# Kernel tuning notes

Measured on AMD Instinct MI355X. Metric: run time of the kernel, lower is better.

Reference implementation:

```python
import jax, jax.numpy as jnp
import numpy as np

LEAKY_SLOPE = 0.01
BN_EPS = 1e-5


def _local_conv(x, w, b, stride):
    # x: [B,C,H,W]; w: [1,O,C,OH,OW,K] (K = kh*kw, kh==kw); b: [1,O,OH,OW]
    sh, sw = stride
    _, O, C, oh, ow, K = w.shape
    k = int(round(K ** 0.5))
    # gather unfold patches: torch .unfold(2,kh,dh).unfold(3,kw,dw) -> last dim ordered (i major, j minor)
    patches = jnp.stack(
        [x[:, :, i:i + sh * oh:sh, j:j + sw * ow:sw] for i in range(k) for j in range(k)],
        axis=-1)  # [B,C,oh,ow,K]
    out = jnp.einsum('bchwk,ochwk->bohw', patches, w[0])
    return out + b  # b broadcasts [1,O,OH,OW]


def _bn_train(x, gamma, beta):
    # BatchNorm2d in training mode: biased batch statistics over (N,H,W)
    m = jnp.mean(x, axis=(0, 2, 3), keepdims=True)
    v = jnp.var(x, axis=(0, 2, 3), keepdims=True)
    return gamma[None, :, None, None] * (x - m) * jax.lax.rsqrt(v + BN_EPS) + beta[None, :, None, None]


def _lrelu(x):
    return jnp.where(x >= 0, x, LEAKY_SLOPE * x)


def _pad1(x):
    return jnp.pad(x, ((0, 0), (0, 0), (1, 1), (1, 1)))


def setup_inputs() -> dict:
    key = jax.random.key(0)
    ks = jax.random.split(key, 16)
    B = 8192
    inp = {
        'image': jax.random.normal(ks[0], (B, 10, 9, 1), jnp.float32),
        'conv1_w': jax.random.normal(ks[1], (64, 1, 2, 2), jnp.float32) * 0.5,
        'conv1_b': jax.random.normal(ks[2], (64,), jnp.float32) * 0.1,
        'lc1_w': jax.random.normal(ks[3], (1, 16, 64, 10, 5, 9), jnp.float32) * 0.05,
        'lc1_b': jax.random.normal(ks[4], (1, 16, 10, 5), jnp.float32) * 0.1,
        'lc2_w': jax.random.normal(ks[5], (1, 8, 16, 11, 6, 4), jnp.float32) * 0.1,
        'lc2_b': jax.random.normal(ks[6], (1, 8, 11, 6), jnp.float32) * 0.1,
        'lc3_w': jax.random.normal(ks[7], (1, 8, 8, 12, 4, 4), jnp.float32) * 0.1,
        'lc3_b': jax.random.normal(ks[8], (1, 8, 12, 4), jnp.float32) * 0.1,
        'gamma1': jax.random.normal(ks[9], (16,), jnp.float32) * 0.1 + 1.0,
        'beta1': jax.random.normal(ks[10], (16,), jnp.float32) * 0.1,
        'gamma2': jax.random.normal(ks[11], (8,), jnp.float32) * 0.1 + 1.0,
        'beta2': jax.random.normal(ks[12], (8,), jnp.float32) * 0.1,
        'gamma3': jax.random.normal(ks[13], (8,), jnp.float32) * 0.1 + 1.0,
        'beta3': jax.random.normal(ks[14], (8,), jnp.float32) * 0.1,
    }
    return inp


def reference(image, conv1_w, conv1_b, lc1_w, lc1_b, lc2_w, lc2_b, lc3_w, lc3_b,
              gamma1, beta1, gamma2, beta2, gamma3, beta3):
    x = jnp.transpose(image, (0, 3, 1, 2))  # [B,1,10,9]
    # Conv2d kernel 2, padding='same' (torch pads extra on right/bottom for even kernels)
    x = jax.lax.conv_general_dilated(
        x, conv1_w, window_strides=(1, 1), padding=[(0, 1), (0, 1)],
        dimension_numbers=('NCHW', 'OIHW', 'NCHW'))
    x = x + conv1_b[None, :, None, None]
    x = _lrelu(x)
    x = _pad1(x)                               # [B,64,12,11]
    x = _local_conv(x, lc1_w, lc1_b, (1, 2))   # [B,16,10,5]
    x = _lrelu(x)
    x = _bn_train(x, gamma1, beta1)
    x = _pad1(x)                               # [B,16,12,7]
    x = _local_conv(x, lc2_w, lc2_b, (1, 1))   # [B,8,11,6]
    x = _lrelu(x)
    x = _bn_train(x, gamma2, beta2)
    x = _pad1(x)                               # [B,8,13,8]
    x = _local_conv(x, lc3_w, lc3_b, (1, 2))   # [B,8,12,4]
    x = _lrelu(x)
    x = _bn_train(x, gamma3, beta3)
    return x.reshape(x.shape[0], -1)           # [B,384]
```

## Files before the change

### kernel.cpp

```cpp
#include <hip/hip_runtime.h>


typedef float  f32x4 __attribute__((ext_vector_type(4)));
typedef float  f32x2 __attribute__((ext_vector_type(2)));
typedef short  bf16x8 __attribute__((ext_vector_type(8)));

union FR  { int4 i4; bf16x8 bf; unsigned u[4]; };
union F2U { f32x2 v; unsigned u[2]; };

#define LRELU(v) fmaxf((v), 0.01f * (v))

static __device__ inline unsigned bfr(float f) {
    unsigned u = __float_as_uint(f);
    return (u + 0x7fffu + ((u >> 16) & 1u)) >> 16;
}
static __device__ inline unsigned short bfr16(float f) { return (unsigned short)bfr(f); }
static __device__ inline float ubf(unsigned lo16) { return __uint_as_float(lo16 << 16); }

#if __has_builtin(__builtin_elementwise_fma)
static __device__ inline f32x2 pk_fma(f32x2 a, f32x2 b, f32x2 c) { return __builtin_elementwise_fma(a, b, c); }
#else
static __device__ inline f32x2 pk_fma(f32x2 a, f32x2 b, f32x2 c) { return a * b + c; }
#endif
static __device__ inline f32x2 pk_lrelu(f32x2 v) {
#if __has_builtin(__builtin_elementwise_max)
    return __builtin_elementwise_max(v, v * 0.01f);
#else
    f32x2 r; r.x = LRELU(v.x); r.y = LRELU(v.y); return r;
#endif
}
static __device__ inline float aload(float* p) {
    return __hip_atomic_load(p, __ATOMIC_RELAXED, __HIP_MEMORY_SCOPE_AGENT);
}

__global__ __launch_bounds__(256) void kB_frags(
    const float* __restrict__ lw1,
    int4* __restrict__ afg1, float* __restrict__ stats)
{
    const int bx = blockIdx.x, tid = threadIdx.x;
    if (bx == 50) { if (tid < 64) stats[tid] = 0.0f; return; }

    const int pos = bx;
    __shared__ float wt[9216];
    for (int e = tid; e < 9216; e += 256) {
        int pair = e / 9, t = e - 9 * pair;
        wt[e] = lw1[pair * 450 + pos * 9 + t];
    }
    __syncthreads();
    for (int e = tid; e < 1152; e += 256) {
        int l = e & 63, ht = e >> 6;
        int h = (ht >= 9) ? 1 : 0, t = ht - 9 * h;
        int q = l >> 4, o = l & 15;
        unsigned uu[4];
        #pragma unroll
        for (int p = 0; p < 4; ++p) {
            int c0 = 32 * h + 8 * q + 2 * p;
            float w0 = wt[(o * 64 + c0) * 9 + t];
            float w1 = wt[(o * 64 + c0 + 1) * 9 + t];
            uu[p] = bfr(w0) | (bfr(w1) << 16);
        }
        int4 st = { (int)uu[0], (int)uu[1], (int)uu[2], (int)uu[3] };
        afg1[pos * 1152 + e] = st;
    }
}

__global__ __launch_bounds__(256) void k1_lc1(
    const float* __restrict__ img,
    const float* __restrict__ cw,
    const float* __restrict__ cb,
    const int4* __restrict__ afg,
    const float* __restrict__ lb,
    unsigned short* __restrict__ y1b,
    float* __restrict__ stats)
{
    __shared__ int4   AfL[1152];
    __shared__ float4 cw4s[64];
    __shared__ float  cbl[64];
    __shared__ float  bl[16];
    __shared__ float  red[32];

    const int pos = blockIdx.y;
    const int oh = pos / 5, ow = pos % 5;
    const int tid = threadIdx.x;
    const int wv = tid >> 6, lane = tid & 63;
    const int lane15 = lane & 15, q = lane >> 4;

    for (int e = tid; e < 1152; e += 256) AfL[e] = afg[pos * 1152 + e];
    if (tid < 64) { cw4s[tid] = ((const float4*)cw)[tid]; cbl[tid] = cb[tid]; }
    if (tid < 16) bl[tid] = lb[tid * 50 + pos];
    if (tid < 32) red[tid] = 0.0f;
    __syncthreads();

    bool km[9];
    #pragma unroll
    for (int i = 0; i < 3; i++)
        #pragma unroll
        for (int j = 0; j < 3; j++) {
            int r = oh + i - 1, c2 = 2 * ow + j - 1;
            km[i * 3 + j] = (r >= 0 && r < 10 && c2 >= 0 && c2 < 9);
        }

    const int sBase = blockIdx.x * 256 + wv * 64;
    float ip[4][16];
    #pragma unroll
    for (int g = 0; g < 4; ++g) {
        const float* ib = img + (size_t)(sBase + g * 16 + lane15) * 90;
        #pragma unroll
        for (int a = 0; a < 4; ++a) {
            int r = oh - 1 + a;
            bool rok = (r >= 0 && r < 10);
            #pragma unroll
            for (int d = 0; d < 4; ++d) {
                int c2 = 2 * ow - 1 + d;
                ip[g][a * 4 + d] = (rok && c2 >= 0 && c2 < 9) ? ib[r * 9 + c2] : 0.0f;
            }
        }
    }

    f32x4 acc[4];
    #pragma unroll
    for (int g = 0; g < 4; ++g) acc[g] = (f32x4){0.f, 0.f, 0.f, 0.f};

    #pragma unroll
    for (int h = 0; h < 2; ++h) {
        f32x2 wx2[4], wy2[4], wz2[4], ww2[4], cb2[4];
        #pragma unroll
        for (int p = 0; p < 4; ++p) {
            float4 wa = cw4s[h * 32 + q * 8 + 2 * p];
            float4 wb = cw4s[h * 32 + q * 8 + 2 * p + 1];
            wx2[p] = (f32x2){wa.x, wb.x};
            wy2[p] = (f32x2){wa.y, wb.y};
            wz2[p] = (f32x2){wa.z, wb.z};
            ww2[p] = (f32x2){wa.w, wb.w};
            cb2[p] = (f32x2){cbl[h * 32 + q * 8 + 2 * p], cbl[h * 32 + q * 8 + 2 * p + 1]};
        }
        #pragma unroll
        for (int t = 0; t < 9; ++t) {
            const int ti = t / 3, tj = t % 3;
            const int i0 = ti * 4 + tj;
            if (km[t]) {
                FR fa; fa.i4 = AfL[(h * 9 + t) * 64 + lane];
                #pragma unroll
                for (int g = 0; g < 4; ++g) {
                    f32x2 s0 = (f32x2)ip[g][i0];
                    f32x2 s1 = (f32x2)ip[g][i0 + 1];
                    f32x2 s2 = (f32x2)ip[g][i0 + 4];
                    f32x2 s3 = (f32x2)ip[g][i0 + 5];
                    FR fb;
                    #pragma unroll
                    for (int p = 0; p < 4; ++p) {
                        f32x2 v = pk_fma(s0, wx2[p], cb2[p]);
                        v = pk_fma(s1, wy2[p], v);
                        v = pk_fma(s2, wz2[p], v);
                        v = pk_fma(s3, ww2[p], v);
                        v = pk_lrelu(v);
                        F2U uu; uu.v = v;
                        fb.u[p] = __builtin_amdgcn_perm(uu.u[1], uu.u[0], 0x07060302u);
                    }
                    acc[g] = __builtin_amdgcn_mfma_f32_16x16x32_bf16(fa.bf, fb.bf, acc[g], 0, 0, 0);
                }
            }
        }
    }

    float so[4] = {0, 0, 0, 0}, sq[4] = {0, 0, 0, 0};
    #pragma unroll
    for (int g = 0; g < 4; ++g)
        #pragma unroll
        for (int r = 0; r < 4; ++r) {
            int o = q * 4 + r;
            float v = acc[g][r] + bl[o];
            v = LRELU(v);
            y1b[(size_t)(o * 50 + pos) * 8192 + sBase + g * 16 + lane15] = bfr16(v);
            so[r] += v; sq[r] += v * v;
        }
    #pragma unroll
    for (int r = 0; r < 4; ++r) {
        #pragma unroll
        for (int m = 1; m < 16; m <<= 1) {
            so[r] += __shfl_xor(so[r], m, 16);
            sq[r] += __shfl_xor(sq[r], m, 16);
        }
        if (lane15 == 0) {
            int o = q * 4 + r;
            atomicAdd(&red[o], so[r]);
            atomicAdd(&red[16 + o], sq[r]);
        }
    }
    __syncthreads();
    if (tid < 32) atomicAdd(&stats[tid], red[tid]);
}

__global__ __launch_bounds__(256) void k2_lc2(
    const unsigned short* __restrict__ y1b,
    const float* __restrict__ lw2, const float* __restrict__ lb2,
    const float* __restrict__ g1, const float* __restrict__ be1,
    unsigned short* __restrict__ y2b, float* __restrict__ stats)
{
    __shared__ float wld[512];
    __shared__ float a1[16], b1[16], bl[8], red[16];

    const int unit = blockIdx.x;
    const int pos = unit >> 3, chunk = unit & 7;
    const int oh = pos / 6, ow = pos % 6;
    const int tid = threadIdx.x, lane = tid & 63;

    if (tid < 128) {
        const float* src = lw2 + tid * 264 + pos * 4;
        int o = tid >> 4, c = tid & 15;
        #pragma unroll
        for (int k = 0; k < 4; k++) wld[c * 32 + k * 8 + o] = src[k];
    }
    if (tid < 16) {
        float m = aload(&stats[tid]) * (1.0f / 409600.0f);
        float v = aload(&stats[16 + tid]) * (1.0f / 409600.0f) - m * m;
        float a = g1[tid] * rsqrtf(v + 1e-5f);
        a1[tid] = a; b1[tid] = be1[tid] - a * m;
        if (tid < 8) bl[tid] = lb2[tid * 66 + pos];
        red[tid] = 0.0f;
    }
    __syncthreads();

    int base[4]; float kmv[4];
    #pragma unroll
    for (int i = 0; i < 2; i++)
        #pragma unroll
        for (int j = 0; j < 2; j++) {
            int r = oh + i - 1, c2 = ow + j - 1;
            bool ok = (r >= 0 && r < 10 && c2 >= 0 && c2 < 5);
            int rc = min(max(r, 0), 9), cc2 = min(max(c2, 0), 4);
            base[i * 2 + j] = rc * 5 + cc2;
            kmv[i * 2 + j] = ok ? 1.0f : 0.0f;
        }

    const int sb = chunk * 1024 + tid * 4;
    float acc[8][4];
    #pragma unroll
    for (int o = 0; o < 8; o++)
        #pragma unroll
        for (int s = 0; s < 4; s++) acc[o][s] = bl[o];

    #pragma unroll 1
    for (int c = 0; c < 16; c++) {
        float av = a1[c], bv = b1[c];
        float p[4][4];
        #pragma unroll
        for (int t = 0; t < 4; t++) {
            float ap = av * kmv[t], bp = bv * kmv[t];
            uint2 U = *(const uint2*)(y1b + (size_t)(c * 50 + base[t]) * 8192 + sb);
            p[t][0] = fmaf(ap, ubf(U.x & 0xffffu), bp);
            p[t][1] = fmaf(ap, __uint_as_float(U.x & 0xffff0000u), bp);
            p[t][2] = fmaf(ap, ubf(U.y & 0xffffu), bp);
            p[t][3] = fmaf(ap, __uint_as_float(U.y & 0xffff0000u), bp);
        }
        const float4* wr = (const float4*)&wld[c * 32];
        #pragma unroll
        for (int t = 0; t < 4; t++) {
            float4 wa = wr[t * 2], wb = wr[t * 2 + 1];
            #pragma unroll
            for (int s = 0; s < 4; s++) {
                float pv = p[t][s];
                acc[0][s] += wa.x * pv; acc[1][s] += wa.y * pv;
                acc[2][s] += wa.z * pv; acc[3][s] += wa.w * pv;
                acc[4][s] += wb.x * pv; acc[5][s] += wb.y * pv;
                acc[6][s] += wb.z * pv; acc[7][s] += wb.w * pv;
            }
        }
    }

    #pragma unroll
    for (int o = 0; o < 8; o++) {
        float v0 = LRELU(acc[o][0]), v1 = LRELU(acc[o][1]);
        float v2 = LRELU(acc[o][2]), v3 = LRELU(acc[o][3]);
        uint2 st = { bfr(v0) | (bfr(v1) << 16), bfr(v2) | (bfr(v3) << 16) };
        *(uint2*)(y2b + (size_t)(o * 66 + pos) * 8192 + sb) = st;
        float sv = v0 + v1 + v2 + v3;
        float sqv = v0 * v0 + v1 * v1 + v2 * v2 + v3 * v3;
        #pragma unroll
        for (int m = 32; m > 0; m >>= 1) {
            sv  += __shfl_xor(sv, m, 64);
            sqv += __shfl_xor(sqv, m, 64);
        }
        if (lane == 0) { atomicAdd(&red[o], sv); atomicAdd(&red[8 + o], sqv); }
    }
    __syncthreads();
    if (tid < 16) atomicAdd(&stats[32 + tid], red[tid]);
}

__global__ __launch_bounds__(256) void k3_lc3(
    const unsigned short* __restrict__ y2b,
    const float* __restrict__ lw3, const float* __restrict__ lb3,
    const float* __restrict__ g2, const float* __restrict__ be2,
    unsigned short* __restrict__ y3b, float* __restrict__ stats)
{
    __shared__ float wld[256];
    __shared__ float a2[8], b2[8], bl[8], red[16];

    const int unit = blockIdx.x;
    const int pos = unit >> 3, chunk = unit & 7;
    const int oh = pos >> 2, ow = pos & 3;
    const int tid = threadIdx.x, lane = tid & 63;

    if (tid < 64) {
        const float* src = lw3 + tid * 192 + pos * 4;
        int o = tid >> 3, c = tid & 7;
        #pragma unroll
        for (int k = 0; k < 4; k++) wld[c * 32 + k * 8 + o] = src[k];
    }
    if (tid < 16) {
        if (tid < 8) {
            float m = aload(&stats[32 + tid]) * (1.0f / 540672.0f);
            float v = aload(&stats[40 + tid]) * (1.0f / 540672.0f) - m * m;
            float a = g2[tid] * rsqrtf(v + 1e-5f);
            a2[tid] = a; b2[tid] = be2[tid] - a * m;
            bl[tid] = lb3[tid * 48 + pos];
        }
        red[tid] = 0.0f;
    }
    __syncthreads();

    int base[4]; float kmv[4];
    #pragma unroll
    for (int i = 0; i < 2; i++)
        #pragma unroll
        for (int j = 0; j < 2; j++) {
            int r = oh + i - 1, c2 = 2 * ow + j - 1;
            bool ok = (r >= 0 && r < 11 && c2 >= 0 && c2 < 6);
            int rc = min(max(r, 0), 10), cc2 = min(max(c2, 0), 5);
            base[i * 2 + j] = rc * 6 + cc2;
            kmv[i * 2 + j] = ok ? 1.0f : 0.0f;
        }

    const int sb = chunk * 1024 + tid * 4;
    float acc[8][4];
    #pragma unroll
    for (int o = 0; o < 8; o++)
        #pragma unroll
        for (int s = 0; s < 4; s++) acc[o][s] = bl[o];

    #pragma unroll 1
    for (int c = 0; c < 8; c++) {
        float av = a2[c], bv = b2[c];
        float p[4][4];
        #pragma unroll
        for (int t = 0; t < 4; t++) {
            float ap = av * kmv[t], bp = bv * kmv[t];
            uint2 U = *(const uint2*)(y2b + (size_t)(c * 66 + base[t]) * 8192 + sb);
            p[t][0] = fmaf(ap, ubf(U.x & 0xffffu), bp);
            p[t][1] = fmaf(ap, __uint_as_float(U.x & 0xffff0000u), bp);
            p[t][2] = fmaf(ap, ubf(U.y & 0xffffu), bp);
            p[t][3] = fmaf(ap, __uint_as_float(U.y & 0xffff0000u), bp);
        }
        const float4* wr = (const float4*)&wld[c * 32];
        #pragma unroll
        for (int t = 0; t < 4; t++) {
            float4 wa = wr[t * 2], wb = wr[t * 2 + 1];
            #pragma unroll
            for (int s = 0; s < 4; s++) {
                float pv = p[t][s];
                acc[0][s] += wa.x * pv; acc[1][s] += wa.y * pv;
                acc[2][s] += wa.z * pv; acc[3][s] += wa.w * pv;
                acc[4][s] += wb.x * pv; acc[5][s] += wb.y * pv;
                acc[6][s] += wb.z * pv; acc[7][s] += wb.w * pv;
            }
        }
    }

    #pragma unroll
    for (int o = 0; o < 8; o++) {
        float v0 = LRELU(acc[o][0]), v1 = LRELU(acc[o][1]);
        float v2 = LRELU(acc[o][2]), v3 = LRELU(acc[o][3]);
        uint2 st = { bfr(v0) | (bfr(v1) << 16), bfr(v2) | (bfr(v3) << 16) };
        *(uint2*)(y3b + (size_t)(o * 48 + pos) * 8192 + sb) = st;
        float sv = v0 + v1 + v2 + v3;
        float sqv = v0 * v0 + v1 * v1 + v2 * v2 + v3 * v3;
        #pragma unroll
        for (int m = 32; m > 0; m >>= 1) {
            sv  += __shfl_xor(sv, m, 64);
            sqv += __shfl_xor(sqv, m, 64);
        }
        if (lane == 0) { atomicAdd(&red[o], sv); atomicAdd(&red[8 + o], sqv); }
    }
    __syncthreads();
    if (tid < 16) atomicAdd(&stats[48 + tid], red[tid]);
}

__global__ __launch_bounds__(256) void k4_out(
    const unsigned short* __restrict__ y3b,
    const float* __restrict__ g3, const float* __restrict__ be3,
    float* __restrict__ stats, float* __restrict__ out)
{
    __shared__ unsigned short tile[64][66];
    __shared__ float a3[8], b3[8];
    const int unit = blockIdx.x;
    const int tid = threadIdx.x;
    const int chunkS = unit & 31, yy = unit >> 5;
    const int ftile = yy >> 2, sub = yy & 3;
    const int fbase = ftile * 64;
    const int sbase = chunkS * 256 + sub * 64;

    if (tid < 8) {
        float m = aload(&stats[48 + tid]) * (1.0f / 393216.0f);
        float v = aload(&stats[56 + tid]) * (1.0f / 393216.0f) - m * m;
        float a = g3[tid] * rsqrtf(v + 1e-5f);
        a3[tid] = a; b3[tid] = be3[tid] - a * m;
    }
    __syncthreads();

    #pragma unroll
    for (int rep = 0; rep < 16; rep++) {
        int idx = rep * 256 + tid;
        int f = idx >> 6, s = idx & 63;
        tile[f][s] = y3b[(size_t)(fbase + f) * 8192 + sbase + s];
    }
    __syncthreads();
    #pragma unroll
    for (int rep = 0; rep < 16; rep++) {
        int idx = rep * 256 + tid;
        int s = idx >> 6, f = idx & 63;
        int ff = fbase + f;
        int o = ff / 48;
        float x = ubf((unsigned)tile[f][s]);
        out[(size_t)(sbase + s) * 384 + ff] = a3[o] * x + b3[o];
    }
}

extern "C" void kernel_launch(void* const* d_in, const int* in_sizes, int n_in,
                              void* d_out, int out_size, void* d_ws, size_t ws_size,
                              hipStream_t stream) {
    const float* image   = (const float*)d_in[0];
    const float* conv1_w = (const float*)d_in[1];
    const float* conv1_b = (const float*)d_in[2];
    const float* lc1_w   = (const float*)d_in[3];
    const float* lc1_b   = (const float*)d_in[4];
    const float* lc2_w   = (const float*)d_in[5];
    const float* lc2_b   = (const float*)d_in[6];
    const float* lc3_w   = (const float*)d_in[7];
    const float* lc3_b   = (const float*)d_in[8];
    const float* gamma1  = (const float*)d_in[9];
    const float* beta1   = (const float*)d_in[10];
    const float* gamma2  = (const float*)d_in[11];
    const float* beta2   = (const float*)d_in[12];
    const float* gamma3  = (const float*)d_in[13];
    const float* beta3   = (const float*)d_in[14];
    float* outp = (float*)d_out;

    char* wsb = (char*)d_ws;
    float*          stats = (float*)wsb;
    unsigned short* y1b   = (unsigned short*)(wsb + 1024);
    unsigned short* y2b   = (unsigned short*)(wsb + 13108224);
    unsigned short* y3b   = (unsigned short*)(wsb + 21758976);
    int4*           afg1  = (int4*)(wsb + 28050432);

    kB_frags<<<dim3(51),     dim3(256), 0, stream>>>(lc1_w, afg1, stats);
    k1_lc1  <<<dim3(32, 50), dim3(256), 0, stream>>>(image, conv1_w, conv1_b,
                                                     afg1, lc1_b, y1b, stats);
    k2_lc2  <<<dim3(528),    dim3(256), 0, stream>>>(y1b, lc2_w, lc2_b,
                                                     gamma1, beta1, y2b, stats);
    k3_lc3  <<<dim3(384),    dim3(256), 0, stream>>>(y2b, lc3_w, lc3_b,
                                                     gamma2, beta2, y3b, stats);
    k4_out  <<<dim3(768),    dim3(256), 0, stream>>>(y3b, gamma3, beta3, stats, outp);
}
```

Baseline: 190.6 us.

## Precompute conv1 activations once into bf16 workspace instead of recomputing per position

```diff
diff --git a/kernel.cpp b/kernel.cpp
--- a/kernel.cpp
+++ b/kernel.cpp
@@ -6,7 +6,6 @@
 typedef short  bf16x8 __attribute__((ext_vector_type(8)));
 
 union FR  { int4 i4; bf16x8 bf; unsigned u[4]; };
-union F2U { f32x2 v; unsigned u[2]; };
 
 #define LRELU(v) fmaxf((v), 0.01f * (v))
 
@@ -33,51 +32,99 @@
     return __hip_atomic_load(p, __ATOMIC_RELAXED, __HIP_MEMORY_SCOPE_AGENT);
 }
 
-__global__ __launch_bounds__(256) void kB_frags(
-    const float* __restrict__ lw1,
-    int4* __restrict__ afg1, float* __restrict__ stats)
-{
-    const int bx = blockIdx.x, tid = threadIdx.x;
-    if (bx == 50) { if (tid < 64) stats[tid] = 0.0f; return; }
-
-    const int pos = bx;
-    __shared__ float wt[9216];
-    for (int e = tid; e < 9216; e += 256) {
-        int pair = e / 9, t = e - 9 * pair;
-        wt[e] = lw1[pair * 450 + pos * 9 + t];
-    }
-    __syncthreads();
-    for (int e = tid; e < 1152; e += 256) {
-        int l = e & 63, ht = e >> 6;
-        int h = (ht >= 9) ? 1 : 0, t = ht - 9 * h;
-        int q = l >> 4, o = l & 15;
-        unsigned uu[4];
-        #pragma unroll
-        for (int p = 0; p < 4; ++p) {
-            int c0 = 32 * h + 8 * q + 2 * p;
-            float w0 = wt[(o * 64 + c0) * 9 + t];
-            float w1 = wt[(o * 64 + c0 + 1) * 9 + t];
-            uu[p] = bfr(w0) | (bfr(w1) << 16);
-        }
-        int4 st = { (int)uu[0], (int)uu[1], (int)uu[2], (int)uu[3] };
-        afg1[pos * 1152 + e] = st;
-    }
-}
-
-__global__ __launch_bounds__(256) void k1_lc1(
-    const float* __restrict__ img,
+union PrepSM { float imgP[16][110]; float wt[9216]; };
+
+__global__ __launch_bounds__(256) void kprep(
+    const float* __restrict__ imgp,
     const float* __restrict__ cw,
     const float* __restrict__ cb,
+    const float* __restrict__ lw1,
+    unsigned* __restrict__ x1u,
+    int4* __restrict__ afg1, float* __restrict__ stats,
+    int nA, int doAux)
+{
+    __shared__ PrepSM sm;
+    const int bx = blockIdx.x, tid = threadIdx.x;
+
+    if (bx < nA) {
+        const int sb = bx * 16;
+        for (int e = tid; e < 1760; e += 256) ((float*)sm.imgP)[e] = 0.0f;
+        __syncthreads();
+        for (int e = tid; e < 1440; e += 256) {
+            int s = e / 90, hw = e - s * 90;
+            int r = hw / 9, c = hw - r * 9;
+            sm.imgP[s][r * 10 + c] = imgp[(size_t)sb * 90 + e];
+        }
+        __syncthreads();
+
+        const int chp = tid & 31, sidx = tid >> 5;
+        const int ch0 = 2 * chp;
+        f32x2 w00 = {cw[ch0 * 4 + 0], cw[ch0 * 4 + 4]};
+        f32x2 w01 = {cw[ch0 * 4 + 1], cw[ch0 * 4 + 5]};
+        f32x2 w10 = {cw[ch0 * 4 + 2], cw[ch0 * 4 + 6]};
+        f32x2 w11 = {cw[ch0 * 4 + 3], cw[ch0 * 4 + 7]};
+        f32x2 bb  = {cb[ch0], cb[ch0 + 1]};
+
+        #pragma unroll
+        for (int ss = 0; ss < 2; ++ss) {
+            const int s = sidx + 8 * ss;
+            const float* ip = sm.imgP[s];
+            unsigned* dst = x1u + (size_t)(sb + s) * 2880 + chp;
+            #pragma unroll 2
+            for (int r = 0; r < 10; ++r) {
+                #pragma unroll
+                for (int c = 0; c < 9; ++c) {
+                    f32x2 v = bb;
+                    v = pk_fma((f32x2)ip[r * 10 + c],      w00, v);
+                    v = pk_fma((f32x2)ip[r * 10 + c + 1],  w01, v);
+                    v = pk_fma((f32x2)ip[r * 10 + c + 10], w10, v);
+                    v = pk_fma((f32x2)ip[r * 10 + c + 11], w11, v);
+                    v = pk_lrelu(v);
+                    dst[(r * 9 + c) * 32] = bfr(v.x) | (bfr(v.y) << 16);
+                }
+            }
+        }
+        return;
+    }
+    if (!doAux) return;
+
+    const int b2 = bx - nA;
+    if (b2 < 50) {
+        const int pos = b2;
+        for (int e = tid; e < 9216; e += 256) {
+            int pair = e / 9, t = e - 9 * pair;
+            sm.wt[e] = lw1[pair * 450 + pos * 9 + t];
+        }
+        __syncthreads();
+        for (int e = tid; e < 1152; e += 256) {
+            int l = e & 63, ht = e >> 6;
+            int h = (ht >= 9) ? 1 : 0, t = ht - 9 * h;
+            int q = l >> 4, o = l & 15;
+            unsigned uu[4];
+            #pragma unroll
+            for (int p = 0; p < 4; ++p) {
+                int c0 = 32 * h + 8 * q + 2 * p;
+                float a0 = sm.wt[(o * 64 + c0) * 9 + t];
+                float a1 = sm.wt[(o * 64 + c0 + 1) * 9 + t];
+                uu[p] = bfr(a0) | (bfr(a1) << 16);
+            }
+            int4 st = { (int)uu[0], (int)uu[1], (int)uu[2], (int)uu[3] };
+            afg1[pos * 1152 + e] = st;
+        }
+    } else if (tid < 64) stats[tid] = 0.0f;
+}
+
+__global__ __launch_bounds__(256) void k1_lc1(
+    const int4* __restrict__ x1v,
     const int4* __restrict__ afg,
     const float* __restrict__ lb,
     unsigned short* __restrict__ y1b,
-    float* __restrict__ stats)
+    float* __restrict__ stats,
+    int sampOff)
 {
-    __shared__ int4   AfL[1152];
-    __shared__ float4 cw4s[64];
-    __shared__ float  cbl[64];
-    __shared__ float  bl[16];
-    __shared__ float  red[32];
+    __shared__ int4  AfL[1152];
+    __shared__ float bl[16];
+    __shared__ float red[32];
 
     const int pos = blockIdx.y;
     const int oh = pos / 5, ow = pos % 5;
@@ -86,77 +133,34 @@
     const int lane15 = lane & 15, q = lane >> 4;
 
     for (int e = tid; e < 1152; e += 256) AfL[e] = afg[pos * 1152 + e];
-    if (tid < 64) { cw4s[tid] = ((const float4*)cw)[tid]; cbl[tid] = cb[tid]; }
     if (tid < 16) bl[tid] = lb[tid * 50 + pos];
     if (tid < 32) red[tid] = 0.0f;
     __syncthreads();
 
-    bool km[9];
-    #pragma unroll
-    for (int i = 0; i < 3; i++)
-        #pragma unroll
-        for (int j = 0; j < 3; j++) {
-            int r = oh + i - 1, c2 = 2 * ow + j - 1;
-            km[i * 3 + j] = (r >= 0 && r < 10 && c2 >= 0 && c2 < 9);
-        }
-
-    const int sBase = blockIdx.x * 256 + wv * 64;
-    float ip[4][16];
-    #pragma unroll
-    for (int g = 0; g < 4; ++g) {
-        const float* ib = img + (size_t)(sBase + g * 16 + lane15) * 90;
-        #pragma unroll
-        for (int a = 0; a < 4; ++a) {
-            int r = oh - 1 + a;
-            bool rok = (r >= 0 && r < 10);
+    const int sLoc = blockIdx.x * 256 + wv * 64;
+    const int sAbs = sampOff + sLoc;
+
+    int sOff[4];
+    #pragma unroll
+    for (int g = 0; g < 4; ++g)
+        sOff[g] = (sLoc + g * 16 + lane15) * 720 + q;
+
+    f32x4 acc[4];
+    #pragma unroll
+    for (int g = 0; g < 4; ++g) acc[g] = (f32x4){0.f, 0.f, 0.f, 0.f};
+
+    #pragma unroll
+    for (int t = 0; t < 9; ++t) {
+        const int ti = t / 3, tj = t % 3;
+        const int r = oh + ti - 1, c2 = 2 * ow + tj - 1;
+        if (r >= 0 && r < 10 && c2 >= 0 && c2 < 9) {
+            const int hw8 = (r * 9 + c2) * 8;
             #pragma unroll
-            for (int d = 0; d < 4; ++d) {
-                int c2 = 2 * ow - 1 + d;
-                ip[g][a * 4 + d] = (rok && c2 >= 0 && c2 < 9) ? ib[r * 9 + c2] : 0.0f;
-            }
-        }
-    }
-
-    f32x4 acc[4];
-    #pragma unroll
-    for (int g = 0; g < 4; ++g) acc[g] = (f32x4){0.f, 0.f, 0.f, 0.f};
-
-    #pragma unroll
-    for (int h = 0; h < 2; ++h) {
-        f32x2 wx2[4], wy2[4], wz2[4], ww2[4], cb2[4];
-        #pragma unroll
-        for (int p = 0; p < 4; ++p) {
-            float4 wa = cw4s[h * 32 + q * 8 + 2 * p];
-            float4 wb = cw4s[h * 32 + q * 8 + 2 * p + 1];
-            wx2[p] = (f32x2){wa.x, wb.x};
-            wy2[p] = (f32x2){wa.y, wb.y};
-            wz2[p] = (f32x2){wa.z, wb.z};
-            ww2[p] = (f32x2){wa.w, wb.w};
-            cb2[p] = (f32x2){cbl[h * 32 + q * 8 + 2 * p], cbl[h * 32 + q * 8 + 2 * p + 1]};
-        }
-        #pragma unroll
-        for (int t = 0; t < 9; ++t) {
-            const int ti = t / 3, tj = t % 3;
-            const int i0 = ti * 4 + tj;
-            if (km[t]) {
+            for (int h = 0; h < 2; ++h) {
                 FR fa; fa.i4 = AfL[(h * 9 + t) * 64 + lane];
                 #pragma unroll
                 for (int g = 0; g < 4; ++g) {
-                    f32x2 s0 = (f32x2)ip[g][i0];
-                    f32x2 s1 = (f32x2)ip[g][i0 + 1];
-                    f32x2 s2 = (f32x2)ip[g][i0 + 4];
-                    f32x2 s3 = (f32x2)ip[g][i0 + 5];
-                    FR fb;
-                    #pragma unroll
-                    for (int p = 0; p < 4; ++p) {
-                        f32x2 v = pk_fma(s0, wx2[p], cb2[p]);
-                        v = pk_fma(s1, wy2[p], v);
-                        v = pk_fma(s2, wz2[p], v);
-                        v = pk_fma(s3, ww2[p], v);
-                        v = pk_lrelu(v);
-                        F2U uu; uu.v = v;
-                        fb.u[p] = __builtin_amdgcn_perm(uu.u[1], uu.u[0], 0x07060302u);
-                    }
+                    FR fb; fb.i4 = x1v[sOff[g] + hw8 + h * 4];
                     acc[g] = __builtin_amdgcn_mfma_f32_16x16x32_bf16(fa.bf, fb.bf, acc[g], 0, 0, 0);
                 }
             }
@@ -171,7 +175,7 @@
             int o = q * 4 + r;
             float v = acc[g][r] + bl[o];
             v = LRELU(v);
-            y1b[(size_t)(o * 50 + pos) * 8192 + sBase + g * 16 + lane15] = bfr16(v);
+            y1b[(size_t)(o * 50 + pos) * 8192 + sAbs + g * 16 + lane15] = bfr16(v);
             so[r] += v; sq[r] += v * v;
         }
     #pragma unroll
@@ -448,16 +452,32 @@
     char* wsb = (char*)d_ws;
     float*          stats = (float*)wsb;
     unsigned short* y1b   = (unsigned short*)(wsb + 1024);
-    unsigned short* y2b   = (unsigned short*)(wsb + 13108224);
-    unsigned short* y3b   = (unsigned short*)(wsb + 21758976);
-    int4*           afg1  = (int4*)(wsb + 28050432);
-
-    kB_frags<<<dim3(51),     dim3(256), 0, stream>>>(lc1_w, afg1, stats);
-    k1_lc1  <<<dim3(32, 50), dim3(256), 0, stream>>>(image, conv1_w, conv1_b,
-                                                     afg1, lc1_b, y1b, stats);
-    k2_lc2  <<<dim3(528),    dim3(256), 0, stream>>>(y1b, lc2_w, lc2_b,
-                                                     gamma1, beta1, y2b, stats);
-    k3_lc3  <<<dim3(384),    dim3(256), 0, stream>>>(y2b, lc3_w, lc3_b,
-                                                     gamma2, beta2, y3b, stats);
-    k4_out  <<<dim3(768),    dim3(256), 0, stream>>>(y3b, gamma3, beta3, stats, outp);
-}
+    int4*           afg1  = (int4*)(wsb + 13108224);
+    char*           x1reg = wsb + 14029824;
+    unsigned short* y2b   = (unsigned short*)(wsb + 14029824);
+    unsigned short* y3b   = (unsigned short*)(wsb + 22680576);
+
+    const size_t bytesPerSamp = 11520;
+    int nPass = 1;
+    if (ws_size < 14029824ul + 8192ul * bytesPerSamp) nPass = 2;
+    if (ws_size < 14029824ul + 4096ul * bytesPerSamp) nPass = 4;
+    if (ws_size < 14029824ul + 2048ul * bytesPerSamp) nPass = 8;
+    const int spp = 8192 / nPass;
+    const int nA  = spp / 16;
+
+    unsigned*   x1u = (unsigned*)x1reg;
+    const int4* x1v = (const int4*)x1reg;
+
+    for (int p = 0; p < nPass; ++p) {
+        const float* imgp = image + (size_t)p * spp * 90;
+        kprep<<<dim3(p == 0 ? nA + 51 : nA), dim3(256), 0, stream>>>(
+            imgp, conv1_w, conv1_b, lc1_w, x1u, afg1, stats, nA, p == 0 ? 1 : 0);
+        k1_lc1<<<dim3(spp / 256, 50), dim3(256), 0, stream>>>(
+            x1v, afg1, lc1_b, y1b, stats, p * spp);
+    }
+    k2_lc2<<<dim3(528), dim3(256), 0, stream>>>(y1b, lc2_w, lc2_b,
+                                                gamma1, beta1, y2b, stats);
+    k3_lc3<<<dim3(384), dim3(256), 0, stream>>>(y2b, lc3_w, lc3_b,
+                                                gamma2, beta2, y3b, stats);
+    k4_out<<<dim3(768), dim3(256), 0, stream>>>(y3b, gamma3, beta3, stats, outp);
+}
```

After: 221.1 us. 1.16x slower.

## Compute conv1 activations once per row in LDS and share across lc1 positions

Applied to the files above, without the earlier changes.

```diff
diff --git a/kernel.cpp b/kernel.cpp
--- a/kernel.cpp
+++ b/kernel.cpp
@@ -6,7 +6,6 @@
 typedef short  bf16x8 __attribute__((ext_vector_type(8)));
 
 union FR  { int4 i4; bf16x8 bf; unsigned u[4]; };
-union F2U { f32x2 v; unsigned u[2]; };
 
 #define LRELU(v) fmaxf((v), 0.01f * (v))
 
@@ -55,16 +54,16 @@
         #pragma unroll
         for (int p = 0; p < 4; ++p) {
             int c0 = 32 * h + 8 * q + 2 * p;
-            float w0 = wt[(o * 64 + c0) * 9 + t];
-            float w1 = wt[(o * 64 + c0 + 1) * 9 + t];
-            uu[p] = bfr(w0) | (bfr(w1) << 16);
+            float a0 = wt[(o * 64 + c0) * 9 + t];
+            float a1 = wt[(o * 64 + c0 + 1) * 9 + t];
+            uu[p] = bfr(a0) | (bfr(a1) << 16);
         }
         int4 st = { (int)uu[0], (int)uu[1], (int)uu[2], (int)uu[3] };
         afg1[pos * 1152 + e] = st;
     }
 }
 
-__global__ __launch_bounds__(256) void k1_lc1(
+__global__ __launch_bounds__(320) void k1_lc1(
     const float* __restrict__ img,
     const float* __restrict__ cw,
     const float* __restrict__ cb,
@@ -73,107 +72,103 @@
     unsigned short* __restrict__ y1b,
     float* __restrict__ stats)
 {
-    __shared__ int4   AfL[1152];
-    __shared__ float4 cw4s[64];
-    __shared__ float  cbl[64];
-    __shared__ float  bl[16];
-    __shared__ float  red[32];
-
-    const int pos = blockIdx.y;
-    const int oh = pos / 5, ow = pos % 5;
+    __shared__ uint4 x1L4[3456];
+    __shared__ float imgP[16][110];
+    __shared__ float blL[80];
+    __shared__ float red[32];
+
+    const int oh = blockIdx.x % 10;
+    const int chunk = blockIdx.x / 10;
+    const int sb = chunk * 16;
     const int tid = threadIdx.x;
-    const int wv = tid >> 6, lane = tid & 63;
+
+    for (int e = tid; e < 1760; e += 320) ((float*)imgP)[e] = 0.0f;
+    if (tid < 80) blL[tid] = lb[(tid & 15) * 50 + oh * 5 + (tid >> 4)];
+    if (tid < 32) red[tid] = 0.0f;
+    __syncthreads();
+    for (int e = tid; e < 1440; e += 320) {
+        int s = e / 90, hw = e - s * 90;
+        int r = hw / 9, c = hw - r * 9;
+        imgP[s][r * 10 + c] = img[(size_t)(sb + s) * 90 + hw];
+    }
+    __syncthreads();
+
+    {
+        const int hq = tid & 7, h = hq >> 2, qq = hq & 3;
+        const int ch0 = h * 32 + qq * 8;
+        f32x2 W00[4], W01[4], W10[4], W11[4], BB[4];
+        #pragma unroll
+        for (int p = 0; p < 4; ++p) {
+            int ca = ch0 + 2 * p, cbn = ca + 1;
+            W00[p] = (f32x2){cw[ca * 4 + 0], cw[cbn * 4 + 0]};
+            W01[p] = (f32x2){cw[ca * 4 + 1], cw[cbn * 4 + 1]};
+            W10[p] = (f32x2){cw[ca * 4 + 2], cw[cbn * 4 + 2]};
+            W11[p] = (f32x2){cw[ca * 4 + 3], cw[cbn * 4 + 3]};
+            BB[p]  = (f32x2){cb[ca], cb[cbn]};
+        }
+        for (int item = tid; item < 3456; item += 320) {
+            int grp = item >> 3;
+            int samp = grp & 15, ic = grp >> 4;
+            int i = ic / 9, c = ic - 9 * i;
+            int rr = min(max(oh - 1 + i, 0), 9);
+            const float* ip = imgP[samp];
+            float i00 = ip[rr * 10 + c],      i01 = ip[rr * 10 + c + 1];
+            float i10 = ip[rr * 10 + c + 10], i11 = ip[rr * 10 + c + 11];
+            unsigned u[4];
+            #pragma unroll
+            for (int p = 0; p < 4; ++p) {
+                f32x2 v = BB[p];
+                v = pk_fma((f32x2)i00, W00[p], v);
+                v = pk_fma((f32x2)i01, W01[p], v);
+                v = pk_fma((f32x2)i10, W10[p], v);
+                v = pk_fma((f32x2)i11, W11[p], v);
+                v = pk_lrelu(v);
+                u[p] = bfr(v.x) | (bfr(v.y) << 16);
+            }
+            int qqs = qq ^ ((samp >> 1) & 3);
+            x1L4[(ic * 2 + h) * 64 + samp * 4 + qqs] = make_uint4(u[0], u[1], u[2], u[3]);
+        }
+    }
+    __syncthreads();
+
+    const int w = tid >> 6;
+    const int lane = tid & 63;
     const int lane15 = lane & 15, q = lane >> 4;
-
-    for (int e = tid; e < 1152; e += 256) AfL[e] = afg[pos * 1152 + e];
-    if (tid < 64) { cw4s[tid] = ((const float4*)cw)[tid]; cbl[tid] = cb[tid]; }
-    if (tid < 16) bl[tid] = lb[tid * 50 + pos];
-    if (tid < 32) red[tid] = 0.0f;
-    __syncthreads();
-
-    bool km[9];
-    #pragma unroll
-    for (int i = 0; i < 3; i++)
-        #pragma unroll
-        for (int j = 0; j < 3; j++) {
-            int r = oh + i - 1, c2 = 2 * ow + j - 1;
-            km[i * 3 + j] = (r >= 0 && r < 10 && c2 >= 0 && c2 < 9);
-        }
-
-    const int sBase = blockIdx.x * 256 + wv * 64;
-    float ip[4][16];
-    #pragma unroll
-    for (int g = 0; g < 4; ++g) {
-        const float* ib = img + (size_t)(sBase + g * 16 + lane15) * 90;
-        #pragma unroll
-        for (int a = 0; a < 4; ++a) {
-            int r = oh - 1 + a;
-            bool rok = (r >= 0 && r < 10);
-            #pragma unroll
-            for (int d = 0; d < 4; ++d) {
-                int c2 = 2 * ow - 1 + d;
-                ip[g][a * 4 + d] = (rok && c2 >= 0 && c2 < 9) ? ib[r * 9 + c2] : 0.0f;
-            }
-        }
-    }
-
-    f32x4 acc[4];
-    #pragma unroll
-    for (int g = 0; g < 4; ++g) acc[g] = (f32x4){0.f, 0.f, 0.f, 0.f};
-
-    #pragma unroll
-    for (int h = 0; h < 2; ++h) {
-        f32x2 wx2[4], wy2[4], wz2[4], ww2[4], cb2[4];
-        #pragma unroll
-        for (int p = 0; p < 4; ++p) {
-            float4 wa = cw4s[h * 32 + q * 8 + 2 * p];
-            float4 wb = cw4s[h * 32 + q * 8 + 2 * p + 1];
-            wx2[p] = (f32x2){wa.x, wb.x};
-            wy2[p] = (f32x2){wa.y, wb.y};
-            wz2[p] = (f32x2){wa.z, wb.z};
-            ww2[p] = (f32x2){wa.w, wb.w};
-            cb2[p] = (f32x2){cbl[h * 32 + q * 8 + 2 * p], cbl[h * 32 + q * 8 + 2 * p + 1]};
-        }
-        #pragma unroll
-        for (int t = 0; t < 9; ++t) {
-            const int ti = t / 3, tj = t % 3;
-            const int i0 = ti * 4 + tj;
-            if (km[t]) {
-                FR fa; fa.i4 = AfL[(h * 9 + t) * 64 + lane];
-                #pragma unroll
-                for (int g = 0; g < 4; ++g) {
-                    f32x2 s0 = (f32x2)ip[g][i0];
-                    f32x2 s1 = (f32x2)ip[g][i0 + 1];
-                    f32x2 s2 = (f32x2)ip[g][i0 + 4];
-                    f32x2 s3 = (f32x2)ip[g][i0 + 5];
-                    FR fb;
-                    #pragma unroll
-                    for (int p = 0; p < 4; ++p) {
-                        f32x2 v = pk_fma(s0, wx2[p], cb2[p]);
-                        v = pk_fma(s1, wy2[p], v);
-                        v = pk_fma(s2, wz2[p], v);
-                        v = pk_fma(s3, ww2[p], v);
-                        v = pk_lrelu(v);
-                        F2U uu; uu.v = v;
-                        fb.u[p] = __builtin_amdgcn_perm(uu.u[1], uu.u[0], 0x07060302u);
-                    }
-                    acc[g] = __builtin_amdgcn_mfma_f32_16x16x32_bf16(fa.bf, fb.bf, acc[g], 0, 0, 0);
-                }
-            }
-        }
-    }
-
-    float so[4] = {0, 0, 0, 0}, sq[4] = {0, 0, 0, 0};
-    #pragma unroll
-    for (int g = 0; g < 4; ++g)
-        #pragma unroll
-        for (int r = 0; r < 4; ++r) {
-            int o = q * 4 + r;
-            float v = acc[g][r] + bl[o];
-            v = LRELU(v);
-            y1b[(size_t)(o * 50 + pos) * 8192 + sBase + g * 16 + lane15] = bfr16(v);
-            so[r] += v; sq[r] += v * v;
-        }
+    const int ow = w, pos = oh * 5 + ow;
+
+    FR fa[18]; int slab[18];
+    #pragma unroll
+    for (int t = 0; t < 9; ++t) {
+        int ti = t / 3, tj = t % 3;
+        int r = oh + ti - 1, c2 = 2 * ow + tj - 1;
+        bool ok = (r >= 0 && r < 10 && c2 >= 0 && c2 < 9);
+        int c2c = min(max(c2, 0), 8);
+        #pragma unroll
+        for (int h = 0; h < 2; ++h) {
+            int s = 2 * t + h;
+            slab[s] = (ti * 9 + c2c) * 2 + h;
+            if (ok) fa[s].i4 = afg[pos * 1152 + (h * 9 + t) * 64 + lane];
+            else    fa[s].i4 = (int4){0, 0, 0, 0};
+        }
+    }
+    const int offB = lane15 * 4 + (q ^ ((lane15 >> 1) & 3));
+
+    f32x4 acc = (f32x4){0.f, 0.f, 0.f, 0.f};
+    #pragma unroll
+    for (int s = 0; s < 18; ++s) {
+        FR fb; fb.i4 = ((const int4*)x1L4)[slab[s] * 64 + offB];
+        acc = __builtin_amdgcn_mfma_f32_16x16x32_bf16(fa[s].bf, fb.bf, acc, 0, 0, 0);
+    }
+
+    float so[4], sq[4];
+    #pragma unroll
+    for (int r = 0; r < 4; ++r) {
+        int o = q * 4 + r;
+        float v = acc[r] + blL[w * 16 + o];
+        v = LRELU(v);
+        y1b[(size_t)(o * 50 + pos) * 8192 + sb + lane15] = bfr16(v);
+        so[r] = v; sq[r] = v * v;
+    }
     #pragma unroll
     for (int r = 0; r < 4; ++r) {
         #pragma unroll
@@ -452,12 +447,12 @@
     unsigned short* y3b   = (unsigned short*)(wsb + 21758976);
     int4*           afg1  = (int4*)(wsb + 28050432);
 
-    kB_frags<<<dim3(51),     dim3(256), 0, stream>>>(lc1_w, afg1, stats);
-    k1_lc1  <<<dim3(32, 50), dim3(256), 0, stream>>>(image, conv1_w, conv1_b,
-                                                     afg1, lc1_b, y1b, stats);
-    k2_lc2  <<<dim3(528),    dim3(256), 0, stream>>>(y1b, lc2_w, lc2_b,
-                                                     gamma1, beta1, y2b, stats);
-    k3_lc3  <<<dim3(384),    dim3(256), 0, stream>>>(y2b, lc3_w, lc3_b,
-                                                     gamma2, beta2, y3b, stats);
-    k4_out  <<<dim3(768),    dim3(256), 0, stream>>>(y3b, gamma3, beta3, stats, outp);
-}
+    kB_frags<<<dim3(51),   dim3(256), 0, stream>>>(lc1_w, afg1, stats);
+    k1_lc1  <<<dim3(5120), dim3(320), 0, stream>>>(image, conv1_w, conv1_b,
+                                                   afg1, lc1_b, y1b, stats);
+    k2_lc2  <<<dim3(528),  dim3(256), 0, stream>>>(y1b, lc2_w, lc2_b,
+                                                   gamma1, beta1, y2b, stats);
+    k3_lc3  <<<dim3(384),  dim3(256), 0, stream>>>(y2b, lc3_w, lc3_b,
+                                                   gamma2, beta2, y3b, stats);
+    k4_out  <<<dim3(768),  dim3(256), 0, stream>>>(y3b, gamma3, beta3, stats, outp);
+}
```

Result: slower. 302.8 us (+58.9%).
